# Performance work log

Hardware: AMD Instinct MI355X
Metric: run time of the kernel (lower is better)

The kernel has to match this reference:

```python
import jax, jax.numpy as jnp
import numpy as np

B, N, D_IN, D_HID, D_OUT, NUM_CLASSES = 2048, 18, 1024, 2048, 1024, 14


def setup_inputs() -> dict:
    key = jax.random.key(0)
    ks = jax.random.split(key, 10)
    stdv1 = 1.0 / np.sqrt(D_HID)
    stdv2 = 1.0 / np.sqrt(D_OUT)
    return {
        "feature": jax.random.normal(ks[0], (B, N, D_IN), dtype=jnp.float32),
        "adj": jax.random.uniform(ks[1], (N, N), dtype=jnp.float32),
        "w1": jax.random.uniform(ks[2], (D_IN, D_HID), minval=-stdv1, maxval=stdv1, dtype=jnp.float32),
        "w2": jax.random.uniform(ks[3], (D_HID, D_OUT), minval=-stdv2, maxval=stdv2, dtype=jnp.float32),
        "ln_w": jnp.ones((D_OUT,), dtype=jnp.float32),
        "ln_b": jnp.zeros((D_OUT,), dtype=jnp.float32),
        "fcn_w": jax.random.normal(ks[4], (NUM_CLASSES, D_OUT), dtype=jnp.float32) * 0.02,
        "fcn_b": jnp.zeros((NUM_CLASSES,), dtype=jnp.float32),
        "fcg_w": jax.random.normal(ks[5], (NUM_CLASSES, D_OUT), dtype=jnp.float32) * 0.02,
        "fcg_b": jnp.zeros((NUM_CLASSES,), dtype=jnp.float32),
    }


def layer_norm(x, w, b, eps=1e-5):
    mu = jnp.mean(x, axis=-1, keepdims=True)
    var = jnp.mean(jnp.square(x - mu), axis=-1, keepdims=True)
    return (x - mu) * jax.lax.rsqrt(var + eps) * w + b


def reference(feature, adj, w1, w2, ln_w, ln_b, fcn_w, fcn_b, fcg_w, fcg_b):
    # GCN layer 1: (adj @ (feature @ W1)), LeakyReLU(0.2)
    x = jnp.einsum("ij,bjh->bih", adj, feature @ w1)            # [B,N,2048]
    x = jax.nn.leaky_relu(x, negative_slope=0.2)
    # GCN layer 2
    x = jnp.einsum("ij,bjd->bid", adj, x @ w2)                  # [B,N,1024]
    # attention-like: feature @ x^T, softmax over last dim, @ feature
    scores = jnp.einsum("bnd,bmd->bnm", feature, x)             # [B,N,N]
    attn = jax.nn.softmax(scores, axis=-1)
    anatomy = jnp.einsum("bnm,bmd->bnd", attn, feature)         # [B,N,1024]
    # residual + LayerNorm (AdaptiveAvgPool2d to same size is identity)
    anatomy = layer_norm(anatomy + feature, ln_w, ln_b)
    node_level = anatomy @ fcn_w.T + fcn_b                       # [B,N,C]
    graph_level = jnp.mean(anatomy, axis=1) @ fcg_w.T + fcg_b    # [B,C]
    return (node_level, graph_level)
```

## Files before the change

### kernel.cpp

```cpp
#include <hip/hip_runtime.h>

typedef unsigned int u32;
typedef _Float16 f16;
typedef __attribute__((ext_vector_type(8))) _Float16 half8;
typedef __attribute__((ext_vector_type(4))) _Float16 half4;
typedef __attribute__((ext_vector_type(4))) float floatx4;

__global__ void transpose_w(const float* __restrict__ in, f16* __restrict__ out,
                            int R, int C) {
  __shared__ f16 t[32][33];
  const int bx = blockIdx.x * 32, by = blockIdx.y * 32;
  const int x = threadIdx.x, y0 = threadIdx.y;
  for (int y = y0; y < 32; y += 8)
    t[y][x] = (f16)in[(size_t)(by + y) * C + bx + x];
  __syncthreads();
  for (int y = y0; y < 32; y += 8)
    out[(size_t)(bx + y) * R + by + x] = t[x][y];
}

__global__ __launch_bounds__(256) void adjmix(const float* __restrict__ F,
                                              const float* __restrict__ adj,
                                              f16* __restrict__ G1) {
  __shared__ float adjs[324];
  for (int i = threadIdx.x; i < 324; i += 256) adjs[i] = adj[i];
  __syncthreads();
  const int d = blockIdx.x * 256 + threadIdx.x;
  const size_t base = (size_t)blockIdx.y * 18432;
  float f[18];
#pragma unroll
  for (int j = 0; j < 18; ++j) f[j] = F[base + j * 1024 + d];
#pragma unroll
  for (int i = 0; i < 18; ++i) {
    float a = 0.f;
#pragma unroll
    for (int j = 0; j < 18; ++j) a += adjs[i * 18 + j] * f[j];
    G1[base + i * 1024 + d] = (f16)a;
  }
}

template <int MODE>
__global__ __launch_bounds__(256) void gemm_bt(const f16* __restrict__ A,
                                               const f16* __restrict__ Bt,
                                               f16* __restrict__ C,
                                               int M, int N, int K) {
  __shared__ __align__(16) f16 As[128 * 64];
  __shared__ __align__(16) f16 Bs[128 * 64];
  const int tid = threadIdx.x;
  const int wave = tid >> 6, lane = tid & 63;
  const int quad = lane >> 4, lrow = lane & 15;
  const size_t m0 = (size_t)blockIdx.x * 128;
  const size_t n0 = (size_t)blockIdx.y * 128;
  const int wm = (wave & 1) * 64, wn = (wave >> 1) * 64;

  floatx4 acc[4][4];
#pragma unroll
  for (int i = 0; i < 4; ++i)
#pragma unroll
    for (int j = 0; j < 4; ++j) acc[i][j] = (floatx4){0.f, 0.f, 0.f, 0.f};

  for (int k0 = 0; k0 < K; k0 += 64) {
#pragma unroll
    for (int g = 0; g < 4; ++g) {
      const int e = g * 256 + tid;
      const int ldsoff = (g * 256 + wave * 64) * 8;
      const f16* ga = A + (m0 + (e >> 3)) * K + k0 + (e & 7) * 8;
      __builtin_amdgcn_global_load_lds(
          (const __attribute__((address_space(1))) void*)ga,
          (__attribute__((address_space(3))) void*)(As + ldsoff), 16, 0, 0);
      const f16* gb = Bt + (n0 + (e >> 3)) * K + k0 + (e & 7) * 8;
      __builtin_amdgcn_global_load_lds(
          (const __attribute__((address_space(1))) void*)gb,
          (__attribute__((address_space(3))) void*)(Bs + ldsoff), 16, 0, 0);
    }
    __syncthreads();
#pragma unroll
    for (int s = 0; s < 2; ++s) {
      half8 a[4], b[4];
#pragma unroll
      for (int i = 0; i < 4; ++i)
        a[i] = *(const half8*)(As + (wm + i * 16 + lrow) * 64 + s * 32 + quad * 8);
#pragma unroll
      for (int j = 0; j < 4; ++j)
        b[j] = *(const half8*)(Bs + (wn + j * 16 + lrow) * 64 + s * 32 + quad * 8);
#pragma unroll
      for (int i = 0; i < 4; ++i)
#pragma unroll
        for (int j = 0; j < 4; ++j)
          acc[i][j] = __builtin_amdgcn_mfma_f32_16x16x32_f16(a[i], b[j], acc[i][j], 0, 0, 0);
    }
    __syncthreads();
  }

#pragma unroll
  for (int i = 0; i < 4; ++i) {
    const size_t rb = m0 + wm + i * 16 + quad * 4;
#pragma unroll
    for (int j = 0; j < 4; ++j) {
      const size_t cb = n0 + wn + j * 16 + lrow;
#pragma unroll
      for (int r = 0; r < 4; ++r) {
        float x = acc[i][j][r];
        if (MODE == 0) x = x > 0.f ? x : 0.2f * x;
        C[(rb + r) * N + cb] = (f16)x;
      }
    }
  }
}

#define HP2 1032
__global__ __launch_bounds__(256, 4) void fused_attn(
    const float* __restrict__ F, const float* __restrict__ adj,
    f16* __restrict__ H2,
    const float* __restrict__ lnw, const float* __restrict__ lnb,
    f16* __restrict__ Msh) {
  __shared__ __align__(16) f16 Hs[18 * HP2];
  __shared__ float Ts[18 * 20];
  __shared__ float Red[324];

  const int tid = threadIdx.x;
  const int lane = tid & 63, wave = tid >> 6;
  const int quad = lane >> 4, l16 = lane & 15;
  const int b = blockIdx.x;
  const float* Fb = F + (size_t)b * 18432;
  f16* Hb = H2 + (size_t)b * 18432;

  for (int i = tid; i < 2304; i += 256) {
    const int r = i >> 7, g = i & 127;
    *(half8*)(Hs + r * HP2 + g * 8) = *(const half8*)(Hb + r * 1024 + g * 8);
  }
  for (int i = tid; i < 324; i += 256) Red[i] = adj[i];
  __syncthreads();

  {
    const int mt = wave >> 1, nt = wave & 1;
    const int arow = min(mt * 16 + l16, 17);
    const int brow = min(nt * 16 + l16, 17);
    const float* ap = Fb + arow * 1024 + quad * 8;
    const f16* bp = Hs + brow * HP2 + quad * 8;
    floatx4 acc = (floatx4){0.f, 0.f, 0.f, 0.f};
    for (int kc = 0; kc < 1024; kc += 32) {
      floatx4 a0 = *(const floatx4*)(ap + kc);
      floatx4 a1 = *(const floatx4*)(ap + kc + 4);
      half8 af;
      af[0] = (f16)a0[0]; af[1] = (f16)a0[1]; af[2] = (f16)a0[2]; af[3] = (f16)a0[3];
      af[4] = (f16)a1[0]; af[5] = (f16)a1[1]; af[6] = (f16)a1[2]; af[7] = (f16)a1[3];
      half8 bf = *(const half8*)(bp + kc);
      acc = __builtin_amdgcn_mfma_f32_16x16x32_f16(af, bf, acc, 0, 0, 0);
    }
    const int row = mt * 16 + quad * 4, col = nt * 16 + l16;
    if (col < 18) {
#pragma unroll
      for (int r = 0; r < 4; ++r)
        if (row + r < 18) Ts[(row + r) * 20 + col] = acc[r];
    }
  }
  __syncthreads();

  if (tid < 18) {
    float t[18], s[18];
#pragma unroll
    for (int j = 0; j < 18; ++j) t[j] = Ts[tid * 20 + j];
    float mx = -3.4e38f;
    for (int m = 0; m < 18; ++m) {
      float a = 0.f;
#pragma unroll
      for (int j = 0; j < 18; ++j) a += t[j] * Red[m * 18 + j];
      s[m] = a; mx = fmaxf(mx, a);
    }
    float sum = 0.f;
    for (int m = 0; m < 18; ++m) { s[m] = __expf(s[m] - mx); sum += s[m]; }
    const float inv = 1.f / sum;
    for (int m = 0; m < 18; ++m) Ts[tid * 20 + m] = s[m] * inv;
  }
  __syncthreads();

  const int d0 = tid;
  floatx4 an[18];
#pragma unroll
  for (int i = 0; i < 18; ++i) an[i] = (floatx4){0.f, 0.f, 0.f, 0.f};
#pragma unroll
  for (int jb = 0; jb < 5; ++jb) {
    const int jn = (jb < 4) ? 4 : 2;
    floatx4 fj[4];
#pragma unroll
    for (int jj = 0; jj < 4; ++jj) {
      if (jj < jn) {
        const float* fp = Fb + (jb * 4 + jj) * 1024 + d0;
        fj[jj] = (floatx4){fp[0], fp[256], fp[512], fp[768]};
        an[jb * 4 + jj] += fj[jj];
      }
    }
#pragma unroll
    for (int i = 0; i < 18; ++i) {
      floatx4 p4 = *(const floatx4*)(Ts + i * 20 + jb * 4);
#pragma unroll
      for (int jj = 0; jj < 4; ++jj)
        if (jj < jn) an[i] += p4[jj] * fj[jj];
    }
  }
  float s[18], ss[18];
#pragma unroll
  for (int i = 0; i < 18; ++i) {
    Hs[i * HP2 + d0] = (f16)an[i][0];
    Hs[i * HP2 + d0 + 256] = (f16)an[i][1];
    Hs[i * HP2 + d0 + 512] = (f16)an[i][2];
    Hs[i * HP2 + d0 + 768] = (f16)an[i][3];
    s[i] = an[i][0] + an[i][1] + an[i][2] + an[i][3];
    ss[i] = an[i][0] * an[i][0] + an[i][1] * an[i][1] +
            an[i][2] * an[i][2] + an[i][3] * an[i][3];
  }
#pragma unroll
  for (int i = 0; i < 18; ++i) {
#pragma unroll
    for (int off = 32; off > 0; off >>= 1) {
      s[i] += __shfl_xor(s[i], off);
      ss[i] += __shfl_xor(ss[i], off);
    }
  }
  if (lane == 0) {
#pragma unroll
    for (int i = 0; i < 18; ++i) {
      Red[wave * 36 + i] = s[i];
      Red[wave * 36 + 18 + i] = ss[i];
    }
  }
  __syncthreads();
  if (tid < 18) {
    const float sv = Red[tid] + Red[36 + tid] + Red[72 + tid] + Red[108 + tid];
    const float sq = Red[18 + tid] + Red[54 + tid] + Red[90 + tid] + Red[126 + tid];
    const float mu = sv * (1.f / 1024.f);
    Red[144 + tid] = mu;
    Red[162 + tid] = rsqrtf(sq * (1.f / 1024.f) - mu * mu + 1e-5f);
  }
  __syncthreads();

  const floatx4 wv = (floatx4){lnw[d0], lnw[d0 + 256], lnw[d0 + 512], lnw[d0 + 768]};
  const floatx4 bv = (floatx4){lnb[d0], lnb[d0 + 256], lnb[d0 + 512], lnb[d0 + 768]};
  floatx4 msum = (floatx4){0.f, 0.f, 0.f, 0.f};
#pragma unroll
  for (int i = 0; i < 18; ++i) {
    const float mu = Red[144 + i], rs = Red[162 + i];
    floatx4 v = (floatx4){(float)Hs[i * HP2 + d0], (float)Hs[i * HP2 + d0 + 256],
                          (float)Hs[i * HP2 + d0 + 512], (float)Hs[i * HP2 + d0 + 768]};
    floatx4 o;
#pragma unroll
    for (int k = 0; k < 4; ++k) o[k] = (v[k] - mu) * rs * wv[k] + bv[k];
    msum += o;
    Hb[i * 1024 + d0] = (f16)o[0];
    Hb[i * 1024 + d0 + 256] = (f16)o[1];
    Hb[i * 1024 + d0 + 512] = (f16)o[2];
    Hb[i * 1024 + d0 + 768] = (f16)o[3];
  }
  f16* mp = Msh + (size_t)b * 1024;
  mp[d0] = (f16)(msum[0] * (1.f / 18.f));
  mp[d0 + 256] = (f16)(msum[1] * (1.f / 18.f));
  mp[d0 + 512] = (f16)(msum[2] * (1.f / 18.f));
  mp[d0 + 768] = (f16)(msum[3] * (1.f / 18.f));
}

__global__ __launch_bounds__(256, 4) void head_gemm(
    const f16* __restrict__ A, const float* __restrict__ W,
    const float* __restrict__ bias, float* __restrict__ out) {
  __shared__ __align__(16) f16 Ws[14 * 1032];
  const int tid = threadIdx.x, lane = tid & 63, wave = tid >> 6;
  const int quad = lane >> 4, l16 = lane & 15;
  for (int i = tid; i < 3584; i += 256) {
    const int r = i >> 8, g = i & 255;
    floatx4 v = *(const floatx4*)(W + r * 1024 + g * 4);
    half4 h;
#pragma unroll
    for (int t = 0; t < 4; ++t) h[t] = (f16)v[t];
    *(half4*)(Ws + r * 1032 + g * 4) = h;
  }
  __syncthreads();
  const f16* bp = Ws + min(l16, 13) * 1032 + quad * 8;
  const float bia = (l16 < 14) ? bias[l16] : 0.f;
  const size_t mbase = (size_t)blockIdx.x * 128 + wave * 32;
#pragma unroll
  for (int mt = 0; mt < 2; ++mt) {
    const size_t m0 = mbase + mt * 16;
    const f16* apx = A + (m0 + l16) * 1024 + quad * 8;
    floatx4 acc = (floatx4){0.f, 0.f, 0.f, 0.f};
    for (int kc = 0; kc < 1024; kc += 32) {
      half8 af = *(const half8*)(apx + kc);
      half8 bf = *(const half8*)(bp + kc);
      acc = __builtin_amdgcn_mfma_f32_16x16x32_f16(af, bf, acc, 0, 0, 0);
    }
    if (l16 < 14) {
      const size_t row = m0 + quad * 4;
#pragma unroll
      for (int r = 0; r < 4; ++r) out[(row + r) * 14 + l16] = acc[r] + bia;
    }
  }
}

extern "C" void kernel_launch(void* const* d_in, const int* in_sizes, int n_in,
                              void* d_out, int out_size, void* d_ws, size_t ws_size,
                              hipStream_t stream) {
  const float* F    = (const float*)d_in[0];
  const float* adj  = (const float*)d_in[1];
  const float* w1   = (const float*)d_in[2];
  const float* w2   = (const float*)d_in[3];
  const float* lnw  = (const float*)d_in[4];
  const float* lnb  = (const float*)d_in[5];
  const float* fcnw = (const float*)d_in[6];
  const float* fcnb = (const float*)d_in[7];
  const float* fcgw = (const float*)d_in[8];
  const float* fcgb = (const float*)d_in[9];

  float* out_node  = (float*)d_out;
  float* out_graph = out_node + (size_t)2048 * 18 * 14;

  char* ws = (char*)d_ws;
  f16* W2t = (f16*)ws;
  f16* W1t = (f16*)(ws + (size_t)(4 << 20));
  char* p8 = ws + (size_t)(8 << 20);

  transpose_w<<<dim3(64, 32), dim3(32, 8), 0, stream>>>(w1, W1t, 1024, 2048);
  transpose_w<<<dim3(32, 64), dim3(32, 8), 0, stream>>>(w2, W2t, 2048, 1024);

  const size_t G1_FULL = 75497472ull;
  const size_t X1_FULL = 150994944ull;
  const size_t NEED_A = (size_t)(8 << 20) + G1_FULL + X1_FULL;
  const size_t NEED_B = (size_t)(8 << 20) + G1_FULL + 9437184ull + 18874368ull + 4194304ull;

  if (ws_size >= NEED_A) {
    f16* G1 = (f16*)p8;
    f16* H2 = (f16*)p8;
    f16* X1 = (f16*)(p8 + G1_FULL);
    f16* Msh = (f16*)(p8 + G1_FULL);
    adjmix<<<dim3(4, 2048), 256, 0, stream>>>(F, adj, G1);
    gemm_bt<0><<<dim3(288, 16), 256, 0, stream>>>(G1, W1t, X1, 36864, 2048, 1024);
    gemm_bt<1><<<dim3(288, 8), 256, 0, stream>>>(X1, W2t, H2, 36864, 1024, 2048);
    fused_attn<<<2048, 256, 0, stream>>>(F, adj, H2, lnw, lnb, Msh);
    head_gemm<<<288, 256, 0, stream>>>(H2, fcnw, fcnb, out_node);
    head_gemm<<<16, 256, 0, stream>>>(Msh, fcgw, fcgb, out_graph);
  } else if (ws_size >= NEED_B) {
    const int CH = 256, MC = CH * 18;
    f16* H2 = (f16*)p8;
    f16* G1c = (f16*)(p8 + G1_FULL);
    f16* X1c = (f16*)(p8 + G1_FULL + 9437184ull);
    f16* Msh = (f16*)(p8 + G1_FULL + 9437184ull + 18874368ull);
    for (int c = 0; c < 8; ++c) {
      const float* Fc = F + (size_t)c * CH * 18432;
      adjmix<<<dim3(4, CH), 256, 0, stream>>>(Fc, adj, G1c);
      gemm_bt<0><<<dim3(36, 16), 256, 0, stream>>>(G1c, W1t, X1c, MC, 2048, 1024);
      gemm_bt<1><<<dim3(36, 8), 256, 0, stream>>>(X1c, W2t,
                                                  H2 + (size_t)c * MC * 1024,
                                                  MC, 1024, 2048);
    }
    fused_attn<<<2048, 256, 0, stream>>>(F, adj, H2, lnw, lnb, Msh);
    head_gemm<<<288, 256, 0, stream>>>(H2, fcnw, fcnb, out_node);
    head_gemm<<<16, 256, 0, stream>>>(Msh, fcgw, fcgb, out_graph);
  } else {
    const int CH = 256, MC = CH * 18;
    f16* G1c = (f16*)p8;
    f16* X1c = (f16*)(p8 + 9437184ull);
    f16* H2c = (f16*)(p8 + 9437184ull + 18874368ull);
    f16* Mshc = (f16*)(p8 + 9437184ull + 18874368ull + 9437184ull);
    for (int c = 0; c < 8; ++c) {
      const float* Fc = F + (size_t)c * CH * 18432;
      adjmix<<<dim3(4, CH), 256, 0, stream>>>(Fc, adj, G1c);
      gemm_bt<0><<<dim3(36, 16), 256, 0, stream>>>(G1c, W1t, X1c, MC, 2048, 1024);
      gemm_bt<1><<<dim3(36, 8), 256, 0, stream>>>(X1c, W2t, H2c, MC, 1024, 2048);
      fused_attn<<<CH, 256, 0, stream>>>(Fc, adj, H2c, lnw, lnb, Mshc);
      head_gemm<<<36, 256, 0, stream>>>(H2c, fcnw, fcnb, out_node + (size_t)c * CH * 252);
      head_gemm<<<2, 256, 0, stream>>>(Mshc, fcgw, fcgb, out_graph + (size_t)c * CH * 14);
    }
  }
}
```

Measured before the change: 901.0 us.

## Replace GEMM with 256x256 tiled, double-buffered, swizzled 8-wave MFMA kernel

The 128x128 four-wave GEMM is replaced by a 256x256-tile, 512-thread kernel. It double-buffers LDS stages via global_load_lds, XOR-swizzles the LDS layout to avoid bank conflicts, and remaps workgroups so each XCD gets a contiguous range. The MFMA work is split into four phases with barriers, s_setprio and explicit waitcnt, so loads of the next K-step overlap compute. The aim is more data reuse per tile and hidden memory latency, at the cost of 128KB LDS per block, high register use (32 accumulators per wave) and fragile hand-written synchronisation.

Result: faster. 770.5 us (-14.5%).

```diff
diff --git a/kernel.cpp b/kernel.cpp
--- a/kernel.cpp
+++ b/kernel.cpp
@@ -5,6 +5,12 @@
 typedef __attribute__((ext_vector_type(8))) _Float16 half8;
 typedef __attribute__((ext_vector_type(4))) _Float16 half4;
 typedef __attribute__((ext_vector_type(4))) float floatx4;
+
+#define BAR() __builtin_amdgcn_s_barrier()
+#define LGKM0() asm volatile("s_waitcnt lgkmcnt(0)" ::: "memory")
+#define VM8() asm volatile("s_waitcnt vmcnt(8)" ::: "memory")
+#define VM0() asm volatile("s_waitcnt vmcnt(0)" ::: "memory")
+#define SETPRIO(x) __builtin_amdgcn_s_setprio(x)
 
 __global__ void transpose_w(const float* __restrict__ in, f16* __restrict__ out,
                             int R, int C) {
@@ -39,69 +45,166 @@
 }
 
 template <int MODE>
-__global__ __launch_bounds__(256) void gemm_bt(const f16* __restrict__ A,
-                                               const f16* __restrict__ Bt,
-                                               f16* __restrict__ C,
-                                               int M, int N, int K) {
-  __shared__ __align__(16) f16 As[128 * 64];
-  __shared__ __align__(16) f16 Bs[128 * 64];
+__global__ __launch_bounds__(512, 2) void gemm8(const f16* __restrict__ A,
+                                                const f16* __restrict__ Bt,
+                                                f16* __restrict__ C,
+                                                int M, int N, int K) {
+  __shared__ __align__(16) f16 lds[65536];
   const int tid = threadIdx.x;
   const int wave = tid >> 6, lane = tid & 63;
-  const int quad = lane >> 4, lrow = lane & 15;
-  const size_t m0 = (size_t)blockIdx.x * 128;
-  const size_t n0 = (size_t)blockIdx.y * 128;
-  const int wm = (wave & 1) * 64, wn = (wave >> 1) * 64;
-
-  floatx4 acc[4][4];
-#pragma unroll
-  for (int i = 0; i < 4; ++i)
+  const int l16 = lane & 15, quad = lane >> 4;
+  const int wr = wave >> 2, wc = wave & 3;
+
+  const int MT = M >> 8;
+  const int nwg = gridDim.x;
+  const int orig = blockIdx.x;
+  const int q = nwg >> 3, r = nwg & 7;
+  const int xcd = orig & 7, idx = orig >> 3;
+  const int wg = (xcd < r) ? xcd * (q + 1) + idx : r * (q + 1) + (xcd - r) * q + idx;
+  const int mt = wg % MT, nt = wg / MT;
+  const size_t m0 = (size_t)mt << 8, n0 = (size_t)nt << 8;
+
+  const f16* gA[4];
+  const f16* gB[4];
+  int ldso[4];
+#pragma unroll
+  for (int g = 0; g < 4; ++g) {
+    const int c = g * 512 + tid;
+    const int row = c >> 3;
+    const int cc = (c & 7) ^ (row & 7);
+    gA[g] = A + (m0 + row) * (size_t)K + cc * 8;
+    gB[g] = Bt + (n0 + row) * (size_t)K + cc * 8;
+    ldso[g] = (g * 512 + (tid & ~63)) * 8;
+  }
+
+  auto STAGE = [&](int buf, int kk) {
+    f16* lA = lds + buf * 32768;
+    f16* lB = lA + 16384;
+#pragma unroll
+    for (int g = 0; g < 4; ++g)
+      __builtin_amdgcn_global_load_lds(
+          (const __attribute__((address_space(1))) void*)(gA[g] + kk),
+          (__attribute__((address_space(3))) void*)(lA + ldso[g]), 16, 0, 0);
+#pragma unroll
+    for (int g = 0; g < 4; ++g)
+      __builtin_amdgcn_global_load_lds(
+          (const __attribute__((address_space(1))) void*)(gB[g] + kk),
+          (__attribute__((address_space(3))) void*)(lB + ldso[g]), 16, 0, 0);
+  };
+
+  const int axor = (l16 & 7) << 3;
+  const int abase = (wr * 128 + l16) * 64 + quad * 8;
+  const int bbase = (wc * 64 + l16) * 64 + quad * 8;
+
+  floatx4 acc[8][4];
+#pragma unroll
+  for (int i = 0; i < 8; ++i)
 #pragma unroll
     for (int j = 0; j < 4; ++j) acc[i][j] = (floatx4){0.f, 0.f, 0.f, 0.f};
 
-  for (int k0 = 0; k0 < K; k0 += 64) {
-#pragma unroll
-    for (int g = 0; g < 4; ++g) {
-      const int e = g * 256 + tid;
-      const int ldsoff = (g * 256 + wave * 64) * 8;
-      const f16* ga = A + (m0 + (e >> 3)) * K + k0 + (e & 7) * 8;
-      __builtin_amdgcn_global_load_lds(
-          (const __attribute__((address_space(1))) void*)ga,
-          (__attribute__((address_space(3))) void*)(As + ldsoff), 16, 0, 0);
-      const f16* gb = Bt + (n0 + (e >> 3)) * K + k0 + (e & 7) * 8;
-      __builtin_amdgcn_global_load_lds(
-          (const __attribute__((address_space(1))) void*)gb,
-          (__attribute__((address_space(3))) void*)(Bs + ldsoff), 16, 0, 0);
-    }
-    __syncthreads();
-#pragma unroll
-    for (int s = 0; s < 2; ++s) {
-      half8 a[4], b[4];
-#pragma unroll
-      for (int i = 0; i < 4; ++i)
-        a[i] = *(const half8*)(As + (wm + i * 16 + lrow) * 64 + s * 32 + quad * 8);
-#pragma unroll
-      for (int j = 0; j < 4; ++j)
-        b[j] = *(const half8*)(Bs + (wn + j * 16 + lrow) * 64 + s * 32 + quad * 8);
-#pragma unroll
-      for (int i = 0; i < 4; ++i)
-#pragma unroll
-        for (int j = 0; j < 4; ++j)
-          acc[i][j] = __builtin_amdgcn_mfma_f32_16x16x32_f16(a[i], b[j], acc[i][j], 0, 0, 0);
-    }
-    __syncthreads();
-  }
-
-#pragma unroll
-  for (int i = 0; i < 4; ++i) {
-    const size_t rb = m0 + wm + i * 16 + quad * 4;
-#pragma unroll
-    for (int j = 0; j < 4; ++j) {
-      const size_t cb = n0 + wn + j * 16 + lrow;
-#pragma unroll
-      for (int r = 0; r < 4; ++r) {
-        float x = acc[i][j][r];
+  const int KT = K >> 6;
+  STAGE(0, 0);
+  STAGE(1, 64);
+  VM8();
+  BAR();
+
+  for (int T = 0; T < KT; ++T) {
+    f16* lA = lds + (T & 1) * 32768;
+    f16* lB = lA + 16384;
+    const bool st = (T + 2 < KT);
+    half8 aF[4][2], bL[2][2], bH[2][2];
+
+#pragma unroll
+    for (int m = 0; m < 4; ++m)
+#pragma unroll
+      for (int s = 0; s < 2; ++s)
+        aF[m][s] = *(const half8*)(lA + ((abase + m * 1024 + s * 32) ^ axor));
+#pragma unroll
+    for (int n = 0; n < 2; ++n)
+#pragma unroll
+      for (int s = 0; s < 2; ++s)
+        bL[n][s] = *(const half8*)(lB + ((bbase + n * 1024 + s * 32) ^ axor));
+    BAR();
+    LGKM0();
+    SETPRIO(1);
+#pragma unroll
+    for (int m = 0; m < 4; ++m)
+#pragma unroll
+      for (int n = 0; n < 2; ++n)
+#pragma unroll
+        for (int s = 0; s < 2; ++s)
+          acc[m][n] = __builtin_amdgcn_mfma_f32_16x16x32_f16(aF[m][s], bL[n][s], acc[m][n], 0, 0, 0);
+    SETPRIO(0);
+    BAR();
+
+#pragma unroll
+    for (int n = 0; n < 2; ++n)
+#pragma unroll
+      for (int s = 0; s < 2; ++s)
+        bH[n][s] = *(const half8*)(lB + ((bbase + (n + 2) * 1024 + s * 32) ^ axor));
+    BAR();
+    LGKM0();
+    SETPRIO(1);
+#pragma unroll
+    for (int m = 0; m < 4; ++m)
+#pragma unroll
+      for (int n = 0; n < 2; ++n)
+#pragma unroll
+        for (int s = 0; s < 2; ++s)
+          acc[m][2 + n] = __builtin_amdgcn_mfma_f32_16x16x32_f16(aF[m][s], bH[n][s], acc[m][2 + n], 0, 0, 0);
+    SETPRIO(0);
+    BAR();
+
+#pragma unroll
+    for (int m = 0; m < 4; ++m)
+#pragma unroll
+      for (int s = 0; s < 2; ++s)
+        aF[m][s] = *(const half8*)(lA + ((abase + (m + 4) * 1024 + s * 32) ^ axor));
+    BAR();
+    LGKM0();
+    SETPRIO(1);
+#pragma unroll
+    for (int m = 0; m < 4; ++m)
+#pragma unroll
+      for (int n = 0; n < 2; ++n)
+#pragma unroll
+        for (int s = 0; s < 2; ++s)
+          acc[4 + m][n] = __builtin_amdgcn_mfma_f32_16x16x32_f16(aF[m][s], bL[n][s], acc[4 + m][n], 0, 0, 0);
+    SETPRIO(0);
+    BAR();
+
+    if (st) STAGE(T & 1, (T + 2) * 64);
+    BAR();
+    SETPRIO(1);
+#pragma unroll
+    for (int m = 0; m < 4; ++m)
+#pragma unroll
+      for (int n = 0; n < 2; ++n)
+#pragma unroll
+        for (int s = 0; s < 2; ++s)
+          acc[4 + m][2 + n] = __builtin_amdgcn_mfma_f32_16x16x32_f16(aF[m][s], bH[n][s], acc[4 + m][2 + n], 0, 0, 0);
+    SETPRIO(0);
+    if (st) {
+      VM8();
+    } else if (T + 1 < KT) {
+      VM0();
+    }
+    BAR();
+  }
+
+  const size_t cr0 = m0 + wr * 128 + quad * 4;
+  const size_t cc0 = n0 + wc * 64 + l16;
+#pragma unroll
+  for (int m = 0; m < 8; ++m) {
+    const size_t rb = cr0 + m * 16;
+#pragma unroll
+    for (int n = 0; n < 4; ++n) {
+      const size_t cb = cc0 + n * 16;
+#pragma unroll
+      for (int rr = 0; rr < 4; ++rr) {
+        float x = acc[m][n][rr];
         if (MODE == 0) x = x > 0.f ? x : 0.2f * x;
-        C[(rb + r) * N + cb] = (f16)x;
+        C[(rb + rr) * N + cb] = (f16)x;
       }
     }
   }
@@ -330,8 +433,8 @@
     f16* X1 = (f16*)(p8 + G1_FULL);
     f16* Msh = (f16*)(p8 + G1_FULL);
     adjmix<<<dim3(4, 2048), 256, 0, stream>>>(F, adj, G1);
-    gemm_bt<0><<<dim3(288, 16), 256, 0, stream>>>(G1, W1t, X1, 36864, 2048, 1024);
-    gemm_bt<1><<<dim3(288, 8), 256, 0, stream>>>(X1, W2t, H2, 36864, 1024, 2048);
+    gemm8<0><<<dim3(1152), 512, 0, stream>>>(G1, W1t, X1, 36864, 2048, 1024);
+    gemm8<1><<<dim3(576), 512, 0, stream>>>(X1, W2t, H2, 36864, 1024, 2048);
     fused_attn<<<2048, 256, 0, stream>>>(F, adj, H2, lnw, lnb, Msh);
     head_gemm<<<288, 256, 0, stream>>>(H2, fcnw, fcnb, out_node);
     head_gemm<<<16, 256, 0, stream>>>(Msh, fcgw, fcgb, out_graph);
@@ -344,10 +447,10 @@
     for (int c = 0; c < 8; ++c) {
       const float* Fc = F + (size_t)c * CH * 18432;
       adjmix<<<dim3(4, CH), 256, 0, stream>>>(Fc, adj, G1c);
-      gemm_bt<0><<<dim3(36, 16), 256, 0, stream>>>(G1c, W1t, X1c, MC, 2048, 1024);
-      gemm_bt<1><<<dim3(36, 8), 256, 0, stream>>>(X1c, W2t,
-                                                  H2 + (size_t)c * MC * 1024,
-                                                  MC, 1024, 2048);
+      gemm8<0><<<dim3(144), 512, 0, stream>>>(G1c, W1t, X1c, MC, 2048, 1024);
+      gemm8<1><<<dim3(72), 512, 0, stream>>>(X1c, W2t,
+                                             H2 + (size_t)c * MC * 1024,
+                                             MC, 1024, 2048);
     }
     fused_attn<<<2048, 256, 0, stream>>>(F, adj, H2, lnw, lnb, Msh);
     head_gemm<<<288, 256, 0, stream>>>(H2, fcnw, fcnb, out_node);
@@ -361,8 +464,8 @@
     for (int c = 0; c < 8; ++c) {
       const float* Fc = F + (size_t)c * CH * 18432;
       adjmix<<<dim3(4, CH), 256, 0, stream>>>(Fc, adj, G1c);
-      gemm_bt<0><<<dim3(36, 16), 256, 0, stream>>>(G1c, W1t, X1c, MC, 2048, 1024);
-      gemm_bt<1><<<dim3(36, 8), 256, 0, stream>>>(X1c, W2t, H2c, MC, 1024, 2048);
+      gemm8<0><<<dim3(144), 512, 0, stream>>>(G1c, W1t, X1c, MC, 2048, 1024);
+      gemm8<1><<<dim3(72), 512, 0, stream>>>(X1c, W2t, H2c, MC, 1024, 2048);
       fused_attn<<<CH, 256, 0, stream>>>(Fc, adj, H2c, lnw, lnb, Mshc);
       head_gemm<<<36, 256, 0, stream>>>(H2c, fcnw, fcnb, out_node + (size_t)c * CH * 252);
       head_gemm<<<2, 256, 0, stream>>>(Mshc, fcgw, fcgb, out_graph + (size_t)c * CH * 14);
```

## Replace GEMM with 256x256 8-wave double-buffered pipelined kernel with XCD remap

Applied to the files above, without the earlier changes.

Swaps the 128x128 single-buffered GEMM for a 256x256-tile, 512-thread kernel. It double-buffers LDS staged via global_load_lds with explicit vmcnt waits, interleaves LDS reads, global prefetch and MFMA clusters under s_setprio, XOR-swizzles LDS to avoid bank conflicts, and remaps block IDs across the 8 XCDs for L2 locality. The aim is to overlap memory with matrix math and raise arithmetic intensity in the two big GCN GEMMs. The cost is higher register pressure (acc[8][4] plus double fragments), a 128 KB LDS footprint, and fragile hand-written wait counts.

Result: slower. 1.116 ms (+23.9%).

```diff
diff --git a/kernel.cpp b/kernel.cpp
--- a/kernel.cpp
+++ b/kernel.cpp
@@ -5,6 +5,12 @@
 typedef __attribute__((ext_vector_type(8))) _Float16 half8;
 typedef __attribute__((ext_vector_type(4))) _Float16 half4;
 typedef __attribute__((ext_vector_type(4))) float floatx4;
+
+#define BAR() __builtin_amdgcn_s_barrier()
+#define VM4() asm volatile("s_waitcnt vmcnt(4)" ::: "memory")
+#define VM2() asm volatile("s_waitcnt vmcnt(2)" ::: "memory")
+#define VM0() asm volatile("s_waitcnt vmcnt(0)" ::: "memory")
+#define SETPRIO(x) __builtin_amdgcn_s_setprio(x)
 
 __global__ void transpose_w(const float* __restrict__ in, f16* __restrict__ out,
                             int R, int C) {
@@ -38,70 +44,175 @@
   }
 }
 
+#define READ_A(DST, BUF, MB)                                             \
+  {                                                                      \
+    _Pragma("unroll") for (int m = 0; m < 4; ++m)                        \
+        _Pragma("unroll") for (int s = 0; s < 2; ++s)                    \
+            DST[m][s] = *(const half8*)(lds + (BUF)*32768 +              \
+                ((abase + ((MB) + m) * 1024 + s * 32) ^ axor));          \
+  }
+#define READ_B(DST, BUF, NB)                                             \
+  {                                                                      \
+    _Pragma("unroll") for (int n = 0; n < 2; ++n)                        \
+        _Pragma("unroll") for (int s = 0; s < 2; ++s)                    \
+            DST[n][s] = *(const half8*)(lds + (BUF)*32768 + 16384 +      \
+                ((bbase + ((NB) + n) * 1024 + s * 32) ^ axor));          \
+  }
+#define MFMA_Q(AA, BB, MO, NO)                                           \
+  {                                                                      \
+    SETPRIO(1);                                                          \
+    _Pragma("unroll") for (int m = 0; m < 4; ++m)                        \
+        _Pragma("unroll") for (int n = 0; n < 2; ++n)                    \
+            _Pragma("unroll") for (int s = 0; s < 2; ++s) acc[(MO) + m]  \
+                [(NO) + n] = __builtin_amdgcn_mfma_f32_16x16x32_f16(     \
+                    AA[m][s], BB[n][s], acc[(MO) + m][(NO) + n], 0, 0,   \
+                    0);                                                  \
+    SETPRIO(0);                                                          \
+  }
+
 template <int MODE>
-__global__ __launch_bounds__(256) void gemm_bt(const f16* __restrict__ A,
-                                               const f16* __restrict__ Bt,
-                                               f16* __restrict__ C,
-                                               int M, int N, int K) {
-  __shared__ __align__(16) f16 As[128 * 64];
-  __shared__ __align__(16) f16 Bs[128 * 64];
+__global__ __launch_bounds__(512, 2) void gemm8(const f16* __restrict__ A,
+                                                const f16* __restrict__ Bt,
+                                                f16* __restrict__ C,
+                                                int M, int N, int K) {
+  __shared__ __align__(16) f16 lds[65536];
   const int tid = threadIdx.x;
   const int wave = tid >> 6, lane = tid & 63;
-  const int quad = lane >> 4, lrow = lane & 15;
-  const size_t m0 = (size_t)blockIdx.x * 128;
-  const size_t n0 = (size_t)blockIdx.y * 128;
-  const int wm = (wave & 1) * 64, wn = (wave >> 1) * 64;
-
-  floatx4 acc[4][4];
-#pragma unroll
-  for (int i = 0; i < 4; ++i)
+  const int l16 = lane & 15, quad = lane >> 4;
+  const int wr = wave >> 2, wc = wave & 3;
+
+  const int MT = M >> 8;
+  const int nwg = gridDim.x;
+  const int orig = blockIdx.x;
+  const int q = nwg >> 3, r = nwg & 7;
+  const int xcd = orig & 7, idx = orig >> 3;
+  const int wg = (xcd < r) ? xcd * (q + 1) + idx : r * (q + 1) + (xcd - r) * q + idx;
+  const int mt = wg % MT, nt = wg / MT;
+  const size_t m0 = (size_t)mt << 8, n0 = (size_t)nt << 8;
+
+  const int prow = tid >> 3;
+  const int pcc = (tid & 7) ^ (prow & 7);
+  const int poff = prow * K + pcc * 8;
+  const int ldsb = (tid & ~63) * 8;
+  const f16* Abase = A + m0 * (size_t)K;
+  const f16* Bbase = Bt + n0 * (size_t)K;
+
+  auto GLO = [&](const f16* gbase, int ldsoff) {
+    __builtin_amdgcn_global_load_lds(
+        (const __attribute__((address_space(1))) void*)(gbase + poff),
+        (__attribute__((address_space(3))) void*)(lds + ldsoff + ldsb), 16, 0, 0);
+  };
+  auto STAGE_A = [&](int buf, int kk, int pair) {
+#pragma unroll
+    for (int g = 2 * pair; g < 2 * pair + 2; ++g)
+      GLO(Abase + (size_t)(g * 64) * K + kk, buf * 32768 + g * 4096);
+  };
+  auto STAGE_B = [&](int buf, int kk, int pair) {
+#pragma unroll
+    for (int g = 2 * pair; g < 2 * pair + 2; ++g)
+      GLO(Bbase + (size_t)(g * 64) * K + kk, buf * 32768 + 16384 + g * 4096);
+  };
+
+  const int axor = (l16 & 7) << 3;
+  const int abase = (wr * 128 + l16) * 64 + quad * 8;
+  const int bbase = (wc * 64 + l16) * 64 + quad * 8;
+
+  floatx4 acc[8][4];
+#pragma unroll
+  for (int i = 0; i < 8; ++i)
 #pragma unroll
     for (int j = 0; j < 4; ++j) acc[i][j] = (floatx4){0.f, 0.f, 0.f, 0.f};
 
-  for (int k0 = 0; k0 < K; k0 += 64) {
-#pragma unroll
-    for (int g = 0; g < 4; ++g) {
-      const int e = g * 256 + tid;
-      const int ldsoff = (g * 256 + wave * 64) * 8;
-      const f16* ga = A + (m0 + (e >> 3)) * K + k0 + (e & 7) * 8;
-      __builtin_amdgcn_global_load_lds(
-          (const __attribute__((address_space(1))) void*)ga,
-          (__attribute__((address_space(3))) void*)(As + ldsoff), 16, 0, 0);
-      const f16* gb = Bt + (n0 + (e >> 3)) * K + k0 + (e & 7) * 8;
-      __builtin_amdgcn_global_load_lds(
-          (const __attribute__((address_space(1))) void*)gb,
-          (__attribute__((address_space(3))) void*)(Bs + ldsoff), 16, 0, 0);
-    }
-    __syncthreads();
-#pragma unroll
-    for (int s = 0; s < 2; ++s) {
-      half8 a[4], b[4];
-#pragma unroll
-      for (int i = 0; i < 4; ++i)
-        a[i] = *(const half8*)(As + (wm + i * 16 + lrow) * 64 + s * 32 + quad * 8);
-#pragma unroll
-      for (int j = 0; j < 4; ++j)
-        b[j] = *(const half8*)(Bs + (wn + j * 16 + lrow) * 64 + s * 32 + quad * 8);
-#pragma unroll
-      for (int i = 0; i < 4; ++i)
-#pragma unroll
-        for (int j = 0; j < 4; ++j)
-          acc[i][j] = __builtin_amdgcn_mfma_f32_16x16x32_f16(a[i], b[j], acc[i][j], 0, 0, 0);
-    }
-    __syncthreads();
-  }
-
-#pragma unroll
-  for (int i = 0; i < 4; ++i) {
-    const size_t rb = m0 + wm + i * 16 + quad * 4;
-#pragma unroll
-    for (int j = 0; j < 4; ++j) {
-      const size_t cb = n0 + wn + j * 16 + lrow;
-#pragma unroll
-      for (int r = 0; r < 4; ++r) {
-        float x = acc[i][j][r];
+  half8 aN[4][2], aF[4][2], bN[2][2], bF[2][2];
+
+  const int KT2 = K >> 7;
+
+  STAGE_A(0, 0, 0);
+  STAGE_A(0, 0, 1);
+  STAGE_B(0, 0, 0);
+  STAGE_B(0, 0, 1);
+  STAGE_A(1, 64, 0);
+  STAGE_A(1, 64, 1);
+  VM4();
+  BAR();
+  READ_A(aN, 0, 0);
+  READ_B(bN, 0, 0);
+  STAGE_B(1, 64, 0);
+
+#pragma unroll 1
+  for (int i = 0; i < KT2; ++i) {
+    const bool nx = (i + 1 < KT2);
+    const int kt0 = i * 128;
+    const int kt1 = kt0 + 64, kt2 = kt0 + 128, kt3 = kt0 + 192;
+
+    READ_A(aF, 0, 4);
+    STAGE_B(1, kt1, 1);
+    BAR();
+    MFMA_Q(aN, bN, 0, 0);
+    BAR();
+
+    READ_B(bF, 0, 2);
+    if (nx) STAGE_A(0, kt2, 0);
+    BAR();
+    MFMA_Q(aF, bN, 4, 0);
+    BAR();
+
+    if (nx) VM2(); else VM0();
+    READ_B(bN, 1, 0);
+    if (nx) STAGE_A(0, kt2, 1);
+    BAR();
+    MFMA_Q(aN, bF, 0, 2);
+    BAR();
+
+    READ_A(aN, 1, 0);
+    if (nx) STAGE_B(0, kt2, 0);
+    BAR();
+    MFMA_Q(aF, bF, 4, 2);
+    BAR();
+
+    READ_A(aF, 1, 4);
+    if (nx) STAGE_B(0, kt2, 1);
+    BAR();
+    MFMA_Q(aN, bN, 0, 0);
+    BAR();
+
+    READ_B(bF, 1, 2);
+    if (nx) STAGE_A(1, kt3, 0);
+    BAR();
+    MFMA_Q(aF, bN, 4, 0);
+    BAR();
+
+    if (nx) {
+      VM2();
+      STAGE_A(1, kt3, 1);
+    }
+    BAR();
+    MFMA_Q(aN, bF, 0, 2);
+    if (nx) READ_A(aN, 0, 0);
+    BAR();
+
+    if (nx) {
+      READ_B(bN, 0, 0);
+      STAGE_B(1, kt3, 0);
+    }
+    BAR();
+    MFMA_Q(aF, bF, 4, 2);
+    BAR();
+  }
+
+  const size_t cr0 = m0 + wr * 128 + quad * 4;
+  const size_t cc0 = n0 + wc * 64 + l16;
+#pragma unroll
+  for (int m = 0; m < 8; ++m) {
+    const size_t rb = cr0 + m * 16;
+#pragma unroll
+    for (int n = 0; n < 4; ++n) {
+      const size_t cb = cc0 + n * 16;
+#pragma unroll
+      for (int rr = 0; rr < 4; ++rr) {
+        float x = acc[m][n][rr];
         if (MODE == 0) x = x > 0.f ? x : 0.2f * x;
-        C[(rb + r) * N + cb] = (f16)x;
+        C[(rb + rr) * N + cb] = (f16)x;
       }
     }
   }
@@ -330,8 +441,8 @@
     f16* X1 = (f16*)(p8 + G1_FULL);
     f16* Msh = (f16*)(p8 + G1_FULL);
     adjmix<<<dim3(4, 2048), 256, 0, stream>>>(F, adj, G1);
-    gemm_bt<0><<<dim3(288, 16), 256, 0, stream>>>(G1, W1t, X1, 36864, 2048, 1024);
-    gemm_bt<1><<<dim3(288, 8), 256, 0, stream>>>(X1, W2t, H2, 36864, 1024, 2048);
+    gemm8<0><<<dim3(1152), 512, 0, stream>>>(G1, W1t, X1, 36864, 2048, 1024);
+    gemm8<1><<<dim3(576), 512, 0, stream>>>(X1, W2t, H2, 36864, 1024, 2048);
     fused_attn<<<2048, 256, 0, stream>>>(F, adj, H2, lnw, lnb, Msh);
     head_gemm<<<288, 256, 0, stream>>>(H2, fcnw, fcnb, out_node);
     head_gemm<<<16, 256, 0, stream>>>(Msh, fcgw, fcgb, out_graph);
@@ -344,10 +455,10 @@
     for (int c = 0; c < 8; ++c) {
       const float* Fc = F + (size_t)c * CH * 18432;
       adjmix<<<dim3(4, CH), 256, 0, stream>>>(Fc, adj, G1c);
-      gemm_bt<0><<<dim3(36, 16), 256, 0, stream>>>(G1c, W1t, X1c, MC, 2048, 1024);
-      gemm_bt<1><<<dim3(36, 8), 256, 0, stream>>>(X1c, W2t,
-                                                  H2 + (size_t)c * MC * 1024,
-                                                  MC, 1024, 2048);
+      gemm8<0><<<dim3(144), 512, 0, stream>>>(G1c, W1t, X1c, MC, 2048, 1024);
+      gemm8<1><<<dim3(72), 512, 0, stream>>>(X1c, W2t,
+                                             H2 + (size_t)c * MC * 1024,
+                                             MC, 1024, 2048);
     }
     fused_attn<<<2048, 256, 0, stream>>>(F, adj, H2, lnw, lnb, Msh);
     head_gemm<<<288, 256, 0, stream>>>(H2, fcnw, fcnb, out_node);
@@ -361,8 +472,8 @@
     for (int c = 0; c < 8; ++c) {
       const float* Fc = F + (size_t)c * CH * 18432;
       adjmix<<<dim3(4, CH), 256, 0, stream>>>(Fc, adj, G1c);
-      gemm_bt<0><<<dim3(36, 16), 256, 0, stream>>>(G1c, W1t, X1c, MC, 2048, 1024);
-      gemm_bt<1><<<dim3(36, 8), 256, 0, stream>>>(X1c, W2t, H2c, MC, 1024, 2048);
+      gemm8<0><<<dim3(144), 512, 0, stream>>>(G1c, W1t, X1c, MC, 2048, 1024);
+      gemm8<1><<<dim3(72), 512, 0, stream>>>(X1c, W2t, H2c, MC, 1024, 2048);
       fused_attn<<<CH, 256, 0, stream>>>(Fc, adj, H2c, lnw, lnb, Mshc);
       head_gemm<<<36, 256, 0, stream>>>(H2c, fcnw, fcnb, out_node + (size_t)c * CH * 252);
       head_gemm<<<2, 256, 0, stream>>>(Mshc, fcgw, fcgb, out_graph + (size_t)c * CH * 14);
```

## Swizzle GEMM LDS layout, remap tiles per XCD, vectorize adjacency mix

Applied to the files above, without the earlier changes.

The fp16 MFMA GEMM now uses an XOR-swizzled LDS layout, where 16-byte chunks are permuted by row, to avoid bank conflicts on the half8 fragment reads. It also uses a 1D grid whose block IDs are remapped so consecutive tiles land on the same XCD, which should improve L2 reuse of shared A/B panels. Per-thread global pointers are precomputed. The adjmix kernel processes 4 floats per thread with vector loads and half4 stores, one block per batch. The swizzle must stay consistent between the global_load_lds writes and the fragment reads, and the tile mapping assumes M and N are multiples of 128.

After: 757.6 us. -15.9%, faster.

```diff
diff --git a/kernel.cpp b/kernel.cpp
--- a/kernel.cpp
+++ b/kernel.cpp
@@ -24,33 +24,62 @@
   __shared__ float adjs[324];
   for (int i = threadIdx.x; i < 324; i += 256) adjs[i] = adj[i];
   __syncthreads();
-  const int d = blockIdx.x * 256 + threadIdx.x;
-  const size_t base = (size_t)blockIdx.y * 18432;
-  float f[18];
-#pragma unroll
-  for (int j = 0; j < 18; ++j) f[j] = F[base + j * 1024 + d];
+  const int d = threadIdx.x * 4;
+  const size_t base = (size_t)blockIdx.x * 18432;
+  floatx4 f[18];
+#pragma unroll
+  for (int j = 0; j < 18; ++j)
+    f[j] = *(const floatx4*)(F + base + j * 1024 + d);
 #pragma unroll
   for (int i = 0; i < 18; ++i) {
-    float a = 0.f;
+    floatx4 a = (floatx4){0.f, 0.f, 0.f, 0.f};
 #pragma unroll
     for (int j = 0; j < 18; ++j) a += adjs[i * 18 + j] * f[j];
-    G1[base + i * 1024 + d] = (f16)a;
+    half4 h;
+#pragma unroll
+    for (int k = 0; k < 4; ++k) h[k] = (f16)a[k];
+    *(half4*)(G1 + base + i * 1024 + d) = h;
   }
 }
 
 template <int MODE>
-__global__ __launch_bounds__(256) void gemm_bt(const f16* __restrict__ A,
+__global__ __launch_bounds__(256) void gemm128(const f16* __restrict__ A,
                                                const f16* __restrict__ Bt,
                                                f16* __restrict__ C,
                                                int M, int N, int K) {
-  __shared__ __align__(16) f16 As[128 * 64];
-  __shared__ __align__(16) f16 Bs[128 * 64];
+  __shared__ __align__(16) f16 As[8192];
+  __shared__ __align__(16) f16 Bs[8192];
   const int tid = threadIdx.x;
   const int wave = tid >> 6, lane = tid & 63;
-  const int quad = lane >> 4, lrow = lane & 15;
-  const size_t m0 = (size_t)blockIdx.x * 128;
-  const size_t n0 = (size_t)blockIdx.y * 128;
-  const int wm = (wave & 1) * 64, wn = (wave >> 1) * 64;
+  const int l16 = lane & 15, quad = lane >> 4;
+  const int wr = wave >> 1, wc = wave & 1;
+
+  const int NT = N >> 7, MT = M >> 7;
+  (void)MT;
+  const int nwg = gridDim.x;
+  const int orig = blockIdx.x;
+  const int q = nwg >> 3, r = nwg & 7;
+  const int xcd = orig & 7, idx = orig >> 3;
+  const int wg = (xcd < r) ? xcd * (q + 1) + idx : r * (q + 1) + (xcd - r) * q + idx;
+  const int nt = wg % NT, mt = wg / NT;
+  const size_t m0 = (size_t)mt << 7, n0 = (size_t)nt << 7;
+
+  const f16* gA[4];
+  const f16* gB[4];
+  int ldso[4];
+#pragma unroll
+  for (int g = 0; g < 4; ++g) {
+    const int c = g * 256 + tid;
+    const int row = c >> 3;
+    const int cc = (c & 7) ^ (row & 7);
+    gA[g] = A + (m0 + row) * (size_t)K + cc * 8;
+    gB[g] = Bt + (n0 + row) * (size_t)K + cc * 8;
+    ldso[g] = (g * 256 + (tid & ~63)) * 8;
+  }
+
+  const int axor = (l16 & 7) << 3;
+  const int abase = (wr * 64 + l16) * 64 + quad * 8;
+  const int bbase = (wc * 64 + l16) * 64 + quad * 8;
 
   floatx4 acc[4][4];
 #pragma unroll
@@ -58,30 +87,29 @@
 #pragma unroll
     for (int j = 0; j < 4; ++j) acc[i][j] = (floatx4){0.f, 0.f, 0.f, 0.f};
 
-  for (int k0 = 0; k0 < K; k0 += 64) {
-#pragma unroll
-    for (int g = 0; g < 4; ++g) {
-      const int e = g * 256 + tid;
-      const int ldsoff = (g * 256 + wave * 64) * 8;
-      const f16* ga = A + (m0 + (e >> 3)) * K + k0 + (e & 7) * 8;
+  const int KT = K >> 6;
+  for (int T = 0; T < KT; ++T) {
+    const int kk = T * 64;
+#pragma unroll
+    for (int g = 0; g < 4; ++g)
       __builtin_amdgcn_global_load_lds(
-          (const __attribute__((address_space(1))) void*)ga,
-          (__attribute__((address_space(3))) void*)(As + ldsoff), 16, 0, 0);
-      const f16* gb = Bt + (n0 + (e >> 3)) * K + k0 + (e & 7) * 8;
+          (const __attribute__((address_space(1))) void*)(gA[g] + kk),
+          (__attribute__((address_space(3))) void*)(As + ldso[g]), 16, 0, 0);
+#pragma unroll
+    for (int g = 0; g < 4; ++g)
       __builtin_amdgcn_global_load_lds(
-          (const __attribute__((address_space(1))) void*)gb,
-          (__attribute__((address_space(3))) void*)(Bs + ldsoff), 16, 0, 0);
-    }
+          (const __attribute__((address_space(1))) void*)(gB[g] + kk),
+          (__attribute__((address_space(3))) void*)(Bs + ldso[g]), 16, 0, 0);
     __syncthreads();
 #pragma unroll
     for (int s = 0; s < 2; ++s) {
       half8 a[4], b[4];
 #pragma unroll
       for (int i = 0; i < 4; ++i)
-        a[i] = *(const half8*)(As + (wm + i * 16 + lrow) * 64 + s * 32 + quad * 8);
+        a[i] = *(const half8*)(As + ((abase + i * 1024 + s * 32) ^ axor));
 #pragma unroll
       for (int j = 0; j < 4; ++j)
-        b[j] = *(const half8*)(Bs + (wn + j * 16 + lrow) * 64 + s * 32 + quad * 8);
+        b[j] = *(const half8*)(Bs + ((bbase + j * 1024 + s * 32) ^ axor));
 #pragma unroll
       for (int i = 0; i < 4; ++i)
 #pragma unroll
@@ -91,17 +119,19 @@
     __syncthreads();
   }
 
+  const size_t cr0 = m0 + wr * 64 + quad * 4;
+  const size_t cc0 = n0 + wc * 64 + l16;
 #pragma unroll
   for (int i = 0; i < 4; ++i) {
-    const size_t rb = m0 + wm + i * 16 + quad * 4;
+    const size_t rb = cr0 + i * 16;
 #pragma unroll
     for (int j = 0; j < 4; ++j) {
-      const size_t cb = n0 + wn + j * 16 + lrow;
-#pragma unroll
-      for (int r = 0; r < 4; ++r) {
-        float x = acc[i][j][r];
+      const size_t cb = cc0 + j * 16;
+#pragma unroll
+      for (int rr = 0; rr < 4; ++rr) {
+        float x = acc[i][j][rr];
         if (MODE == 0) x = x > 0.f ? x : 0.2f * x;
-        C[(rb + r) * N + cb] = (f16)x;
+        C[(rb + rr) * N + cb] = (f16)x;
       }
     }
   }
@@ -329,9 +359,9 @@
     f16* H2 = (f16*)p8;
     f16* X1 = (f16*)(p8 + G1_FULL);
     f16* Msh = (f16*)(p8 + G1_FULL);
-    adjmix<<<dim3(4, 2048), 256, 0, stream>>>(F, adj, G1);
-    gemm_bt<0><<<dim3(288, 16), 256, 0, stream>>>(G1, W1t, X1, 36864, 2048, 1024);
-    gemm_bt<1><<<dim3(288, 8), 256, 0, stream>>>(X1, W2t, H2, 36864, 1024, 2048);
+    adjmix<<<dim3(2048), 256, 0, stream>>>(F, adj, G1);
+    gemm128<0><<<dim3(4608), 256, 0, stream>>>(G1, W1t, X1, 36864, 2048, 1024);
+    gemm128<1><<<dim3(2304), 256, 0, stream>>>(X1, W2t, H2, 36864, 1024, 2048);
     fused_attn<<<2048, 256, 0, stream>>>(F, adj, H2, lnw, lnb, Msh);
     head_gemm<<<288, 256, 0, stream>>>(H2, fcnw, fcnb, out_node);
     head_gemm<<<16, 256, 0, stream>>>(Msh, fcgw, fcgb, out_graph);
@@ -343,11 +373,11 @@
     f16* Msh = (f16*)(p8 + G1_FULL + 9437184ull + 18874368ull);
     for (int c = 0; c < 8; ++c) {
       const float* Fc = F + (size_t)c * CH * 18432;
-      adjmix<<<dim3(4, CH), 256, 0, stream>>>(Fc, adj, G1c);
-      gemm_bt<0><<<dim3(36, 16), 256, 0, stream>>>(G1c, W1t, X1c, MC, 2048, 1024);
-      gemm_bt<1><<<dim3(36, 8), 256, 0, stream>>>(X1c, W2t,
-                                                  H2 + (size_t)c * MC * 1024,
-                                                  MC, 1024, 2048);
+      adjmix<<<dim3(CH), 256, 0, stream>>>(Fc, adj, G1c);
+      gemm128<0><<<dim3(576), 256, 0, stream>>>(G1c, W1t, X1c, MC, 2048, 1024);
+      gemm128<1><<<dim3(288), 256, 0, stream>>>(X1c, W2t,
+                                                H2 + (size_t)c * MC * 1024,
+                                                MC, 1024, 2048);
     }
     fused_attn<<<2048, 256, 0, stream>>>(F, adj, H2, lnw, lnb, Msh);
     head_gemm<<<288, 256, 0, stream>>>(H2, fcnw, fcnb, out_node);
@@ -360,9 +390,9 @@
     f16* Mshc = (f16*)(p8 + 9437184ull + 18874368ull + 9437184ull);
     for (int c = 0; c < 8; ++c) {
       const float* Fc = F + (size_t)c * CH * 18432;
-      adjmix<<<dim3(4, CH), 256, 0, stream>>>(Fc, adj, G1c);
-      gemm_bt<0><<<dim3(36, 16), 256, 0, stream>>>(G1c, W1t, X1c, MC, 2048, 1024);
-      gemm_bt<1><<<dim3(36, 8), 256, 0, stream>>>(X1c, W2t, H2c, MC, 1024, 2048);
+      adjmix<<<dim3(CH), 256, 0, stream>>>(Fc, adj, G1c);
+      gemm128<0><<<dim3(576), 256, 0, stream>>>(G1c, W1t, X1c, MC, 2048, 1024);
+      gemm128<1><<<dim3(288), 256, 0, stream>>>(X1c, W2t, H2c, MC, 1024, 2048);
       fused_attn<<<CH, 256, 0, stream>>>(Fc, adj, H2c, lnw, lnb, Mshc);
       head_gemm<<<36, 256, 0, stream>>>(H2c, fcnw, fcnb, out_node + (size_t)c * CH * 252);
       head_gemm<<<2, 256, 0, stream>>>(Mshc, fcgw, fcgb, out_graph + (size_t)c * CH * 14);
```
